# Kernel tuning notes

Measured on AMD Instinct MI355X. Metric: run time of the kernel, lower is better.

Reference implementation:

```python
import jax, jax.numpy as jnp
import numpy as np

B, L, D, NH, NP = 8, 4096, 384, 8, 4


def setup_inputs() -> dict:
    key = jax.random.key(0)
    ks = jax.random.split(key, 16)
    s = 1.0 / np.sqrt(D)
    f32 = jnp.float32
    inp = {
        'query': jax.random.normal(ks[0], (B, L, D), f32),
        'key':   jax.random.normal(ks[1], (B, L, D), f32),
        'value': jax.random.normal(ks[2], (B, L, D), f32),
        # linear weights stored as [in, out]; x @ W + b
        'Wq': jax.random.normal(ks[3], (D, D), f32) * s,
        'bq': jnp.zeros((D,), f32),
        'Wk': jax.random.normal(ks[4], (D, D), f32) * s,
        'bk': jnp.zeros((D,), f32),
        'Wv': jax.random.normal(ks[5], (D, D), f32) * s,
        'bv': jnp.zeros((D,), f32),
        'Woff': jax.random.normal(ks[6], (D, NH * NP * 2), f32) * s,
        'boff': jnp.zeros((NH * NP * 2,), f32),
        'Wwt': jax.random.normal(ks[7], (D, NH * NP), f32) * s,
        'bwt': jnp.zeros((NH * NP,), f32),
        'Wo': jax.random.normal(ks[8], (D, D), f32) * s,
        'bo': jnp.zeros((D,), f32),
        'num_heads': NH,
        'n_points': NP,
    }
    return inp


def reference(query, key, value, Wq, bq, Wk, bk, Wv, bv, Woff, boff, Wwt, bwt, Wo, bo, num_heads, n_points):
    Bq, Lq, Dm = query.shape
    Lk = key.shape[1]
    Lv = value.shape[1]
    hd = Dm // num_heads
    h = w = int(round(np.sqrt(Lk)))  # original: feature_size = int(sqrt(Lk))

    q = query @ Wq + bq          # computed as in original (only its reshape is used via output path)
    k = key @ Wk + bk            # faithful: k_proj is computed but unused downstream
    v = value @ Wv + bv

    # offsets [B, nH, Lq, nP, 2] and softmax point weights [B, nH, Lq, nP]
    off = (query @ Woff + boff).reshape(Bq, Lq, num_heads, n_points, 2).transpose(0, 2, 1, 3, 4)
    wt = jax.nn.softmax((query @ Wwt + bwt).reshape(Bq, Lq, num_heads, n_points).transpose(0, 2, 1, 3), axis=-1)

    # reference grid: ref[...,0] = x (tiled over rows), ref[...,1] = y (repeated over cols)
    yy = jnp.linspace(0.0, 1.0, h)
    xx = jnp.linspace(0.0, 1.0, w)
    gy, gx = jnp.meshgrid(yy, xx, indexing='ij')
    ref = jnp.stack([gx.reshape(-1), gy.reshape(-1)], axis=-1)  # [L, 2]

    loc = jnp.clip(ref[None, None, :, None, :] + off, 0.0, 1.0)  # [B,nH,Lq,nP,2]
    # NOTE: faithful to source, which multiplies component 0 by (h-1) (its 'h' coord)
    ph = loc[..., 0] * (h - 1)   # row pixel coord, in [0, h-1]
    pw = loc[..., 1] * (w - 1)   # col pixel coord, in [0, w-1]

    y0 = jnp.floor(ph)
    x0 = jnp.floor(pw)
    wy = (ph - y0)[..., None]
    wx = (pw - x0)[..., None]
    y0i = y0.astype(jnp.int32)
    x0i = x0.astype(jnp.int32)
    y1i = jnp.minimum(y0i + 1, h - 1)
    x1i = jnp.minimum(x0i + 1, w - 1)

    vh = v.reshape(Bq, Lv, num_heads, hd).transpose(0, 2, 1, 3)  # [B,nH,Lv,hd]

    def gather(yi, xi):
        idx = (yi * w + xi).reshape(Bq, num_heads, Lq * n_points, 1)
        return jnp.take_along_axis(vh, idx, axis=2).reshape(Bq, num_heads, Lq, n_points, hd)

    # bilinear sample (align_corners=True; coords in-range so zero-padding never triggers)
    sampled = ((1 - wy) * ((1 - wx) * gather(y0i, x0i) + wx * gather(y0i, x1i))
               + wy * ((1 - wx) * gather(y1i, x0i) + wx * gather(y1i, x1i)))

    out = jnp.einsum('bhlp,bhlpd->bhld', wt, sampled)  # weighted point aggregation
    out = out.transpose(0, 2, 1, 3).reshape(Bq, Lq, Dm)
    return out @ Wo + bo  # dropout is identity in eval mode
```

## Files before the change

### kernel.cpp

```cpp
#include <hip/hip_runtime.h>
#include <hip/hip_bf16.h>
#include <stdint.h>

using bf16 = __hip_bfloat16;

typedef __attribute__((ext_vector_type(8))) short short8;
typedef __attribute__((ext_vector_type(4))) float float4v;

namespace {
constexpr int kL  = 4096;
constexpr int kD  = 384;
constexpr int kGW = 64;
constexpr int kM  = 32768;
constexpr int kAP = 392;

constexpr size_t nValue = (size_t)kM * kD;
constexpr size_t nW     = (size_t)kD * kD;
constexpr size_t nWcat  = (size_t)96 * kD;

constexpr size_t oWvt  = 0;
constexpr size_t oWot  = oWvt  + nW * 2;
constexpr size_t oWch  = oWot  + nW * 2;
constexpr size_t oWcl  = oWch  + nWcat * 2;
constexpr size_t oBcat = oWcl  + nWcat * 2;
constexpr size_t oVB   = (oBcat + 96 * 4 + 255) & ~size_t(255);
constexpr size_t oProj = oVB   + nValue * 2;
}

__device__ __forceinline__ void load_lds_16(const void* g, void* l) {
  __builtin_amdgcn_global_load_lds((const __attribute__((address_space(1))) void*)g,
                                   (__attribute__((address_space(3))) void*)l,
                                   16, 0, 0);
}

__device__ __forceinline__ short bf16bits(float f) {
  bf16 h = __float2bfloat16(f);
  return *reinterpret_cast<short*>(&h);
}

__device__ __forceinline__ float bf16raw2f(unsigned short u) {
  union { unsigned int i; float f; } c;
  c.i = ((unsigned int)u) << 16;
  return c.f;
}

__device__ __forceinline__ short8 pack_hi8(const float4& f0, const float4& f1) {
  short8 hx;
  hx[0] = bf16bits(f0.x); hx[1] = bf16bits(f0.y);
  hx[2] = bf16bits(f0.z); hx[3] = bf16bits(f0.w);
  hx[4] = bf16bits(f1.x); hx[5] = bf16bits(f1.y);
  hx[6] = bf16bits(f1.z); hx[7] = bf16bits(f1.w);
  return hx;
}

__device__ __forceinline__ void pack_hilo8(const float4& f0, const float4& f1,
                                           short8& hx, short8& lx) {
  const float fv[8] = {f0.x, f0.y, f0.z, f0.w, f1.x, f1.y, f1.z, f1.w};
  #pragma unroll
  for (int q = 0; q < 8; ++q) {
    const bf16 h = __float2bfloat16(fv[q]);
    hx[q] = *reinterpret_cast<const short*>(&h);
    const bf16 lo = __float2bfloat16(fv[q] - __bfloat162float(h));
    lx[q] = *reinterpret_cast<const short*>(&lo);
  }
}

__global__ void prep_kernel(const float* __restrict__ Wv,
                            const float* __restrict__ Wo,
                            const float* __restrict__ Woff,
                            const float* __restrict__ Wwt,
                            const float* __restrict__ boff,
                            const float* __restrict__ bwt,
                            bf16* __restrict__ Wvt, bf16* __restrict__ Wot,
                            bf16* __restrict__ Wch, bf16* __restrict__ Wcl,
                            float* __restrict__ bcat)
{
  size_t i = (size_t)blockIdx.x * 256 + threadIdx.x;
  if (i < nW) {
    const int n = (int)(i / kD), k = (int)(i % kD);
    Wvt[i] = __float2bfloat16(Wv[(size_t)k * kD + n]);
    return;
  }
  i -= nW;
  if (i < nW) {
    const int n = (int)(i / kD), k = (int)(i % kD);
    Wot[i] = __float2bfloat16(Wo[(size_t)k * kD + n]);
    return;
  }
  i -= nW;
  if (i < nWcat) {
    const int n = (int)(i / kD), k = (int)(i % kD);
    const float val = (n < 64) ? Woff[(size_t)k * 64 + n] : Wwt[(size_t)k * 32 + (n - 64)];
    const bf16 h = __float2bfloat16(val);
    Wch[i] = h;
    Wcl[i] = __float2bfloat16(val - __bfloat162float(h));
    return;
  }
  i -= nWcat;
  if (i < 96) bcat[i] = (i < 64) ? boff[i] : bwt[i - 64];
}

__device__ __forceinline__
void vgemm_body(char* smem, int bid,
                const float* __restrict__ A, const bf16* __restrict__ Bt,
                const float* __restrict__ bias, bf16* __restrict__ Cout)
{
  bf16* sA = (bf16*)smem;
  bf16* sB = (bf16*)(smem + 16384);
  const int tid  = threadIdx.x;
  const int lane = tid & 63;
  const int wave = tid >> 6;
  const int bm = bid / 3, bn = bid % 3;
  const int m0 = bm * 128, n0 = bn * 128;
  const int wm = (wave >> 1) * 64, wn = (wave & 1) * 64;
  const int r16 = lane & 15, quad = lane >> 4;

  float4v acc[4][4];
  #pragma unroll
  for (int i = 0; i < 4; ++i)
    #pragma unroll
    for (int j = 0; j < 4; ++j) acc[i][j] = (float4v){0.f, 0.f, 0.f, 0.f};

  for (int kt = 0; kt < 6; ++kt) {
    const int k0 = kt * 64;
    #pragma unroll
    for (int r = 0; r < 4; ++r) {
      const int e = tid + r * 256;
      const int row = e >> 3, j = e & 7;
      const float* src = A + (size_t)(m0 + row) * kD + k0 + j * 8;
      const float4 f0 = *(const float4*)src;
      const float4 f1 = *(const float4*)(src + 4);
      const int jw = j ^ (row & 7);
      *(short8*)(sA + row * 64 + jw * 8) = pack_hi8(f0, f1);
    }
    #pragma unroll
    for (int r = 0; r < 4; ++r) {
      const int c = tid + r * 256;
      const int row = c >> 3, j = c & 7;
      const int js = j ^ (row & 7);
      load_lds_16(Bt + (size_t)(n0 + row) * kD + k0 + js * 8, (char*)sB + c * 16);
    }
    __syncthreads();
    #pragma unroll
    for (int ks = 0; ks < 2; ++ks) {
      short8 av[4], bv[4];
      #pragma unroll
      for (int i = 0; i < 4; ++i) {
        const int row = wm + i * 16 + r16;
        const int ch = (ks * 4 + quad) ^ (row & 7);
        av[i] = *(const short8*)(sA + row * 64 + ch * 8);
      }
      #pragma unroll
      for (int j = 0; j < 4; ++j) {
        const int row = wn + j * 16 + r16;
        const int ch = (ks * 4 + quad) ^ (row & 7);
        bv[j] = *(const short8*)(sB + row * 64 + ch * 8);
      }
      #pragma unroll
      for (int i = 0; i < 4; ++i)
        #pragma unroll
        for (int j = 0; j < 4; ++j)
          acc[i][j] = __builtin_amdgcn_mfma_f32_16x16x32_bf16(av[i], bv[j], acc[i][j], 0, 0, 0);
    }
    __syncthreads();
  }

  #pragma unroll
  for (int j = 0; j < 4; ++j) {
    const int col = n0 + wn + j * 16 + r16;
    const float bj = bias[col];
    #pragma unroll
    for (int i = 0; i < 4; ++i) {
      const int mbase = m0 + wm + i * 16 + quad * 4;
      #pragma unroll
      for (int r = 0; r < 4; ++r)
        Cout[(size_t)(mbase + r) * kD + col] = __float2bfloat16(acc[i][j][r] + bj);
    }
  }
}

__device__ __forceinline__
void proj_body(char* smem, int bid,
               const float* __restrict__ Q,
               const bf16* __restrict__ WhT, const bf16* __restrict__ WlT,
               const float* __restrict__ bc, float* __restrict__ proj)
{
  bf16* sAh = (bf16*)smem;
  bf16* sAl = (bf16*)(smem + 8192);
  bf16* sBh = (bf16*)(smem + 16384);
  bf16* sBl = (bf16*)(smem + 22528);
  const int tid  = threadIdx.x;
  const int lane = tid & 63;
  const int wave = tid >> 6;
  const int m0 = bid * 128;
  const int wm = (wave >> 1) * 64, wn = (wave & 1) * 48;
  const int r16 = lane & 15, quad = lane >> 4;

  float4v acc[4][3];
  #pragma unroll
  for (int i = 0; i < 4; ++i)
    #pragma unroll
    for (int j = 0; j < 3; ++j) acc[i][j] = (float4v){0.f, 0.f, 0.f, 0.f};

  for (int kt = 0; kt < 12; ++kt) {
    const int k0 = kt * 32;
    #pragma unroll
    for (int r = 0; r < 2; ++r) {
      const int e = tid + r * 256;
      const int row = e >> 2, j = e & 3;
      const float* src = Q + (size_t)(m0 + row) * kD + k0 + j * 8;
      const float4 f0 = *(const float4*)src;
      const float4 f1 = *(const float4*)(src + 4);
      short8 hx, lx;
      pack_hilo8(f0, f1, hx, lx);
      const int jw = j ^ (row & 3);
      *(short8*)(sAh + row * 32 + jw * 8) = hx;
      *(short8*)(sAl + row * 32 + jw * 8) = lx;
    }
    {
      int c = tid;
      int row = c >> 2, j = c & 3, js = j ^ (row & 3);
      load_lds_16(WhT + (size_t)row * kD + k0 + js * 8, (char*)sBh + c * 16);
      if (tid < 128) {
        c = tid + 256;
        row = c >> 2; j = c & 3; js = j ^ (row & 3);
        load_lds_16(WhT + (size_t)row * kD + k0 + js * 8, (char*)sBh + c * 16);
      } else {
        c = tid - 128;
        row = c >> 2; j = c & 3; js = j ^ (row & 3);
        load_lds_16(WlT + (size_t)row * kD + k0 + js * 8, (char*)sBl + c * 16);
      }
      c = tid + 128;
      row = c >> 2; j = c & 3; js = j ^ (row & 3);
      load_lds_16(WlT + (size_t)row * kD + k0 + js * 8, (char*)sBl + c * 16);
    }
    __syncthreads();

    short8 avh[4], avl[4];
    #pragma unroll
    for (int i = 0; i < 4; ++i) {
      const int row = wm + i * 16 + r16;
      const int ch = quad ^ (row & 3);
      avh[i] = *(const short8*)(sAh + row * 32 + ch * 8);
      avl[i] = *(const short8*)(sAl + row * 32 + ch * 8);
    }
    #pragma unroll
    for (int j = 0; j < 3; ++j) {
      const int row = wn + j * 16 + r16;
      const int ch = quad ^ (row & 3);
      const short8 bvh = *(const short8*)(sBh + row * 32 + ch * 8);
      const short8 bvl = *(const short8*)(sBl + row * 32 + ch * 8);
      #pragma unroll
      for (int i = 0; i < 4; ++i) {
        acc[i][j] = __builtin_amdgcn_mfma_f32_16x16x32_bf16(avh[i], bvh, acc[i][j], 0, 0, 0);
        acc[i][j] = __builtin_amdgcn_mfma_f32_16x16x32_bf16(avh[i], bvl, acc[i][j], 0, 0, 0);
        acc[i][j] = __builtin_amdgcn_mfma_f32_16x16x32_bf16(avl[i], bvh, acc[i][j], 0, 0, 0);
      }
    }
    __syncthreads();
  }

  #pragma unroll
  for (int j = 0; j < 3; ++j) {
    const int col = wn + j * 16 + r16;
    const float bj = bc[col];
    #pragma unroll
    for (int i = 0; i < 4; ++i) {
      const int mbase = m0 + wm + i * 16 + quad * 4;
      #pragma unroll
      for (int r = 0; r < 4; ++r)
        proj[(size_t)(mbase + r) * 96 + col] = acc[i][j][r] + bj;
    }
  }
}

__global__ __launch_bounds__(256)
void fat_kernel(const float* __restrict__ value, const bf16* __restrict__ Wvt,
                const float* __restrict__ bv,    bf16* __restrict__ vB,
                const float* __restrict__ Q,     const bf16* __restrict__ Wch,
                const bf16* __restrict__ Wcl,    const float* __restrict__ bcat,
                float* __restrict__ proj)
{
  __shared__ __align__(16) char smem[32768];
  const int pb = blockIdx.x;
  if (pb < 256) {
    proj_body(smem, pb, Q, Wch, Wcl, bcat, proj);
  } else {
    vgemm_body(smem, pb - 256, value, Wvt, bv, vB);
  }
}

__global__ __launch_bounds__(512)
void tail_kernel(const float* __restrict__ proj, const bf16* __restrict__ v,
                 const bf16* __restrict__ Wot, const float* __restrict__ bo,
                 float* __restrict__ out)
{
  __shared__ __align__(16) char smem[66560];
  bf16*   sAgg  = (bf16*)smem;
  int4*   scoff = (int4*)(smem + 50176);
  float4* scw   = (float4*)(smem + 58368);

  const int raw   = blockIdx.x;
  const int chunk = (raw & 7) * 64 + (raw >> 3);
  const int m0    = chunk * 64;
  const int b     = m0 >> 12;
  const int l0    = m0 & 4095;
  const int t     = threadIdx.x;

  for (int ct = 0; ct < 4; ++ct) {
    const int tok0 = ct * 16;
    {
      const int tl = t >> 5, pt = t & 31;
      const int tok = tok0 + tl;
      const int l   = l0 + tok;
      const float* pb_ = proj + (size_t)(m0 + tok) * 96;
      const float2 off = *(const float2*)(pb_ + 2 * pt);
      const int h = pt >> 2, p = pt & 3;
      const float4 lg = *(const float4*)(pb_ + 64 + h * 4);
      const float g[4] = {lg.x, lg.y, lg.z, lg.w};
      const float mx = fmaxf(fmaxf(g[0], g[1]), fmaxf(g[2], g[3]));
      float e[4], sum = 0.f;
      #pragma unroll
      for (int jj = 0; jj < 4; ++jj) { e[jj] = expf(g[jj] - mx); sum += e[jj]; }
      const float wt = e[p] / sum;
      const float refx = (float)(l & 63) * (1.0f / 63.0f);
      const float refy = (float)(l >> 6) * (1.0f / 63.0f);
      const float locx = fminf(fmaxf(refx + off.x, 0.f), 1.f);
      const float locy = fminf(fmaxf(refy + off.y, 0.f), 1.f);
      const float ph = locx * 63.0f;
      const float pw = locy * 63.0f;
      const float fy = floorf(ph), fx = floorf(pw);
      const int y0 = (int)fy, x0 = (int)fx;
      const int y1 = min(y0 + 1, 63), x1 = min(x0 + 1, 63);
      const float wy = ph - fy, wx = pw - fx;
      scoff[tl * 32 + pt] = make_int4((y0 * kGW + x0) * kD, (y0 * kGW + x1) * kD,
                                      (y1 * kGW + x0) * kD, (y1 * kGW + x1) * kD);
      scw[tl * 32 + pt] = make_float4(wt * (1.f - wy) * (1.f - wx), wt * (1.f - wy) * wx,
                                      wt * wy * (1.f - wx),         wt * wy * wx);
    }
    __syncthreads();
    #pragma unroll
    for (int it = 0; it < 3; ++it) {
      const int task = t + it * 512;
      const int tl = task / 96;
      const int q  = task - tl * 96;
      const int h  = q / 12;
      const int col = q * 4;
      const unsigned short* vb = (const unsigned short*)(v + (size_t)b * kL * kD + col);
      float4v acc = (float4v){0.f, 0.f, 0.f, 0.f};
      #pragma unroll
      for (int p = 0; p < 4; ++p) {
        const int4   o = scoff[tl * 32 + h * 4 + p];
        const float4 w = scw  [tl * 32 + h * 4 + p];
        const ushort4 u0 = *(const ushort4*)(vb + o.x);
        const ushort4 u1 = *(const ushort4*)(vb + o.y);
        const ushort4 u2 = *(const ushort4*)(vb + o.z);
        const ushort4 u3 = *(const ushort4*)(vb + o.w);
        acc[0] += w.x * bf16raw2f(u0.x) + w.y * bf16raw2f(u1.x)
                + w.z * bf16raw2f(u2.x) + w.w * bf16raw2f(u3.x);
        acc[1] += w.x * bf16raw2f(u0.y) + w.y * bf16raw2f(u1.y)
                + w.z * bf16raw2f(u2.y) + w.w * bf16raw2f(u3.y);
        acc[2] += w.x * bf16raw2f(u0.z) + w.y * bf16raw2f(u1.z)
                + w.z * bf16raw2f(u2.z) + w.w * bf16raw2f(u3.z);
        acc[3] += w.x * bf16raw2f(u0.w) + w.y * bf16raw2f(u1.w)
                + w.z * bf16raw2f(u2.w) + w.w * bf16raw2f(u3.w);
      }
      ushort4 ou;
      ou.x = (unsigned short)bf16bits(acc[0]);
      ou.y = (unsigned short)bf16bits(acc[1]);
      ou.z = (unsigned short)bf16bits(acc[2]);
      ou.w = (unsigned short)bf16bits(acc[3]);
      *(ushort4*)(sAgg + (size_t)(tok0 + tl) * kAP + col) = ou;
    }
    __syncthreads();
  }

  const int lane = t & 63, wave = t >> 6;
  const int r16 = lane & 15, quad = lane >> 4;
  const int wn = wave * 48;
  float4v acc2[4][3];
  #pragma unroll
  for (int i = 0; i < 4; ++i)
    #pragma unroll
    for (int j = 0; j < 3; ++j) acc2[i][j] = (float4v){0.f, 0.f, 0.f, 0.f};

  const bf16* Bbase = Wot + (size_t)(wn + r16) * kD + quad * 8;

  #pragma unroll
  for (int kt = 0; kt < 12; ++kt) {
    const int k0 = kt * 32;
    short8 av[4];
    #pragma unroll
    for (int i = 0; i < 4; ++i)
      av[i] = *(const short8*)(sAgg + (size_t)(i * 16 + r16) * kAP + k0 + quad * 8);
    #pragma unroll
    for (int j = 0; j < 3; ++j) {
      const short8 bvj = *(const short8*)(Bbase + (size_t)(j * 16) * kD + k0);
      #pragma unroll
      for (int i = 0; i < 4; ++i)
        acc2[i][j] = __builtin_amdgcn_mfma_f32_16x16x32_bf16(av[i], bvj, acc2[i][j], 0, 0, 0);
    }
  }

  #pragma unroll
  for (int j = 0; j < 3; ++j) {
    const int col = wn + j * 16 + r16;
    const float bj = bo[col];
    #pragma unroll
    for (int i = 0; i < 4; ++i) {
      const int mb = m0 + i * 16 + quad * 4;
      #pragma unroll
      for (int r = 0; r < 4; ++r)
        out[(size_t)(mb + r) * kD + col] = acc2[i][j][r] + bj;
    }
  }
}

extern "C" void kernel_launch(void* const* d_in, const int* in_sizes, int n_in,
                              void* d_out, int out_size, void* d_ws, size_t ws_size,
                              hipStream_t stream)
{
  const float* query = (const float*)d_in[0];
  const float* value = (const float*)d_in[2];
  const float* Wv    = (const float*)d_in[7];
  const float* bv    = (const float*)d_in[8];
  const float* Woff  = (const float*)d_in[9];
  const float* boff  = (const float*)d_in[10];
  const float* Wwt   = (const float*)d_in[11];
  const float* bwt   = (const float*)d_in[12];
  const float* Wo    = (const float*)d_in[13];
  const float* bo    = (const float*)d_in[14];
  float* out = (float*)d_out;

  char* ws = (char*)d_ws;
  bf16*  Wvt  = (bf16*)(ws + oWvt);
  bf16*  Wot  = (bf16*)(ws + oWot);
  bf16*  Wch  = (bf16*)(ws + oWch);
  bf16*  Wcl  = (bf16*)(ws + oWcl);
  float* bcat = (float*)(ws + oBcat);
  bf16*  vB   = (bf16*)(ws + oVB);
  float* proj = (float*)(ws + oProj);

  const size_t prepN = nW + nW + nWcat + 96;
  prep_kernel<<<dim3((unsigned)((prepN + 255) / 256)), 256, 0, stream>>>(
      Wv, Wo, Woff, Wwt, boff, bwt, Wvt, Wot, Wch, Wcl, bcat);

  fat_kernel<<<dim3(256 + 768), 256, 0, stream>>>(
      value, Wvt, bv, vB, query, Wch, Wcl, bcat, proj);

  tail_kernel<<<dim3(512), 512, 0, stream>>>(proj, vB, Wot, bo, out);
}
```

Baseline: 267.5 us.

## Double-buffer value GEMM LDS tiles with BK=32 and change swizzle pattern

```diff
diff --git a/kernel.cpp b/kernel.cpp
--- a/kernel.cpp
+++ b/kernel.cpp
@@ -106,7 +106,7 @@
                 const float* __restrict__ bias, bf16* __restrict__ Cout)
 {
   bf16* sA = (bf16*)smem;
-  bf16* sB = (bf16*)(smem + 16384);
+  char* sBB = smem + 16384;
   const int tid  = threadIdx.x;
   const int lane = tid & 63;
   const int wave = tid >> 6;
@@ -121,48 +121,63 @@
     #pragma unroll
     for (int j = 0; j < 4; ++j) acc[i][j] = (float4v){0.f, 0.f, 0.f, 0.f};
 
-  for (int kt = 0; kt < 6; ++kt) {
-    const int k0 = kt * 64;
-    #pragma unroll
-    for (int r = 0; r < 4; ++r) {
-      const int e = tid + r * 256;
-      const int row = e >> 3, j = e & 7;
-      const float* src = A + (size_t)(m0 + row) * kD + k0 + j * 8;
-      const float4 f0 = *(const float4*)src;
-      const float4 f1 = *(const float4*)(src + 4);
-      const int jw = j ^ (row & 7);
-      *(short8*)(sA + row * 64 + jw * 8) = pack_hi8(f0, f1);
-    }
-    #pragma unroll
-    for (int r = 0; r < 4; ++r) {
-      const int c = tid + r * 256;
-      const int row = c >> 3, j = c & 7;
-      const int js = j ^ (row & 7);
-      load_lds_16(Bt + (size_t)(n0 + row) * kD + k0 + js * 8, (char*)sB + c * 16);
-    }
-    __syncthreads();
-    #pragma unroll
-    for (int ks = 0; ks < 2; ++ks) {
-      short8 av[4], bv[4];
-      #pragma unroll
-      for (int i = 0; i < 4; ++i) {
-        const int row = wm + i * 16 + r16;
-        const int ch = (ks * 4 + quad) ^ (row & 7);
-        av[i] = *(const short8*)(sA + row * 64 + ch * 8);
-      }
-      #pragma unroll
-      for (int j = 0; j < 4; ++j) {
-        const int row = wn + j * 16 + r16;
-        const int ch = (ks * 4 + quad) ^ (row & 7);
-        bv[j] = *(const short8*)(sB + row * 64 + ch * 8);
-      }
-      #pragma unroll
-      for (int i = 0; i < 4; ++i)
-        #pragma unroll
-        for (int j = 0; j < 4; ++j)
-          acc[i][j] = __builtin_amdgcn_mfma_f32_16x16x32_bf16(av[i], bv[j], acc[i][j], 0, 0, 0);
-    }
-    __syncthreads();
+  const int e0 = tid, e1 = tid + 256;
+  const int rA0 = e0 >> 2, gA0 = e0 & 3;
+  const int rA1 = e1 >> 2, gA1 = e1 & 3;
+  const int wA0 = rA0 * 32 + (gA0 ^ ((rA0 >> 1) & 3)) * 8;
+  const int wA1 = rA1 * 32 + (gA1 ^ ((rA1 >> 1) & 3)) * 8;
+  const int sBc0 = (gA0 ^ ((rA0 >> 1) & 3)) * 8;
+  const int sBc1 = (gA1 ^ ((rA1 >> 1) & 3)) * 8;
+
+  float4 f00, f01, f10, f11;
+  auto loadA = [&](int k0) {
+    const float* s0 = A + (size_t)(m0 + rA0) * kD + k0 + gA0 * 8;
+    f00 = *(const float4*)s0; f01 = *(const float4*)(s0 + 4);
+    const float* s1 = A + (size_t)(m0 + rA1) * kD + k0 + gA1 * 8;
+    f10 = *(const float4*)s1; f11 = *(const float4*)(s1 + 4);
+  };
+  auto writeA = [&](int buf) {
+    *(short8*)(sA + buf * 4096 + wA0) = pack_hi8(f00, f01);
+    *(short8*)(sA + buf * 4096 + wA1) = pack_hi8(f10, f11);
+  };
+  auto stageB = [&](int k0, int buf) {
+    load_lds_16(Bt + (size_t)(n0 + rA0) * kD + k0 + sBc0, sBB + buf * 8192 + e0 * 16);
+    load_lds_16(Bt + (size_t)(n0 + rA1) * kD + k0 + sBc1, sBB + buf * 8192 + e1 * 16);
+  };
+
+  loadA(0);
+  stageB(0, 0);
+  writeA(0);
+  __syncthreads();
+
+  for (int kt = 0; kt < 12; ++kt) {
+    const int cur = kt & 1, nxt = cur ^ 1;
+    if (kt < 11) {
+      loadA((kt + 1) * 32);
+      stageB((kt + 1) * 32, nxt);
+    }
+    const bf16* sAc = sA + cur * 4096;
+    const bf16* sBc = (const bf16*)(sBB + cur * 8192);
+    short8 av[4], bv[4];
+    #pragma unroll
+    for (int i = 0; i < 4; ++i) {
+      const int row = wm + i * 16 + r16;
+      av[i] = *(const short8*)(sAc + row * 32 + (quad ^ ((row >> 1) & 3)) * 8);
+    }
+    #pragma unroll
+    for (int j = 0; j < 4; ++j) {
+      const int row = wn + j * 16 + r16;
+      bv[j] = *(const short8*)(sBc + row * 32 + (quad ^ ((row >> 1) & 3)) * 8);
+    }
+    #pragma unroll
+    for (int i = 0; i < 4; ++i)
+      #pragma unroll
+      for (int j = 0; j < 4; ++j)
+        acc[i][j] = __builtin_amdgcn_mfma_f32_16x16x32_bf16(av[i], bv[j], acc[i][j], 0, 0, 0);
+    if (kt < 11) {
+      writeA(nxt);
+      __syncthreads();
+    }
   }
 
   #pragma unroll
@@ -213,25 +228,25 @@
       const float4 f1 = *(const float4*)(src + 4);
       short8 hx, lx;
       pack_hilo8(f0, f1, hx, lx);
-      const int jw = j ^ (row & 3);
+      const int jw = j ^ ((row >> 1) & 3);
       *(short8*)(sAh + row * 32 + jw * 8) = hx;
       *(short8*)(sAl + row * 32 + jw * 8) = lx;
     }
     {
       int c = tid;
-      int row = c >> 2, j = c & 3, js = j ^ (row & 3);
+      int row = c >> 2, j = c & 3, js = j ^ ((row >> 1) & 3);
       load_lds_16(WhT + (size_t)row * kD + k0 + js * 8, (char*)sBh + c * 16);
       if (tid < 128) {
         c = tid + 256;
-        row = c >> 2; j = c & 3; js = j ^ (row & 3);
+        row = c >> 2; j = c & 3; js = j ^ ((row >> 1) & 3);
         load_lds_16(WhT + (size_t)row * kD + k0 + js * 8, (char*)sBh + c * 16);
       } else {
         c = tid - 128;
-        row = c >> 2; j = c & 3; js = j ^ (row & 3);
+        row = c >> 2; j = c & 3; js = j ^ ((row >> 1) & 3);
         load_lds_16(WlT + (size_t)row * kD + k0 + js * 8, (char*)sBl + c * 16);
       }
       c = tid + 128;
-      row = c >> 2; j = c & 3; js = j ^ (row & 3);
+      row = c >> 2; j = c & 3; js = j ^ ((row >> 1) & 3);
       load_lds_16(WlT + (size_t)row * kD + k0 + js * 8, (char*)sBl + c * 16);
     }
     __syncthreads();
@@ -240,14 +255,14 @@
     #pragma unroll
     for (int i = 0; i < 4; ++i) {
       const int row = wm + i * 16 + r16;
-      const int ch = quad ^ (row & 3);
+      const int ch = quad ^ ((row >> 1) & 3);
       avh[i] = *(const short8*)(sAh + row * 32 + ch * 8);
       avl[i] = *(const short8*)(sAl + row * 32 + ch * 8);
     }
     #pragma unroll
     for (int j = 0; j < 3; ++j) {
       const int row = wn + j * 16 + r16;
-      const int ch = quad ^ (row & 3);
+      const int ch = quad ^ ((row >> 1) & 3);
       const short8 bvh = *(const short8*)(sBh + row * 32 + ch * 8);
       const short8 bvl = *(const short8*)(sBl + row * 32 + ch * 8);
       #pragma unroll
```

Result: no change. 264.9 us (-1.0%).
